# Performance work log

Measured on AMD Instinct MI355X. Metric: run time of the kernel, lower is better.

The kernel has to match this reference:

```python
import jax, jax.numpy as jnp
import numpy as np

B, N, D = 4, 2048, 1024
THRESHOLD_FACTOR = 1.25


def setup_inputs() -> dict:
    key = jax.random.key(0)
    ks = jax.random.split(key, 8)
    s = 0.02  # init scale matching torch.randn * 0.02
    return {
        "hidden_states": jax.random.normal(ks[0], (B, N, D), jnp.float32),
        "Wq": jax.random.normal(ks[1], (D, D), jnp.float32) * s,
        "bq": jnp.zeros((D,), jnp.float32),
        "Wk": jax.random.normal(ks[2], (D, D), jnp.float32) * s,
        "bk": jnp.zeros((D,), jnp.float32),
        "Wv": jax.random.normal(ks[3], (D, D), jnp.float32) * s,
        "bv": jnp.zeros((D,), jnp.float32),
        "Wo": jax.random.normal(ks[4], (D, D), jnp.float32) * s,
        "bo": jnp.zeros((D,), jnp.float32),
        "Wtq": jax.random.normal(ks[5], (2, D), jnp.float32) * s,  # nn.Linear(D, 2)
        "btq": jnp.zeros((2,), jnp.float32),
        "Wfq": jax.random.normal(ks[6], (D, 2), jnp.float32) * s,  # HebbianLinear(2, D)
        "bfq": jnp.zeros((D,), jnp.float32),
    }


def _linear(x, W, b):
    return x @ W.T + b


def reference(hidden_states, Wq, bq, Wk, bk, Wv, bv, Wo, bo, Wtq, btq, Wfq, bfq):
    d = hidden_states.shape[-1]
    q = _linear(hidden_states, Wq, bq)
    k = _linear(hidden_states, Wk, bk)
    v = _linear(hidden_states, Wv, bv)
    scores = jnp.einsum('bid,bjd->bij', q, k) / jnp.sqrt(jnp.asarray(d, scores_dtype := q.dtype))

    # PhaseAwareBinaryAttention on 2-d quantum projection
    qp = _linear(hidden_states, Wtq, btq)            # [B, N, 2]
    diff = qp[:, :, None, :] - qp[:, None, :, :]      # [B, N, N, 2]
    dist_sq = jnp.sum(diff * diff, axis=-1)           # [B, N, N]
    phase_diff = jnp.arctan2(diff[..., 1], diff[..., 0])
    forward_bias = 0.5 * (1.0 + jnp.cos(phase_diff))
    mean_dist = jnp.mean(dist_sq, axis=(-1, -2), keepdims=True)
    std_dist = jnp.std(dist_sq, axis=(-1, -2), keepdims=True, ddof=1)  # torch unbiased std
    threshold = mean_dist + THRESHOLD_FACTOR * std_dist
    n = dist_sq.shape[-1]
    causal = jnp.tril(jnp.ones((n, n), bool))
    valid = (dist_sq <= threshold) & causal[None]
    binary_attn = valid.astype(scores.dtype) * forward_bias

    masked = jnp.where(binary_attn == 0, -jnp.inf, scores)
    weights = jax.nn.softmax(masked, axis=-1)
    context = jnp.einsum('bij,bjd->bid', weights, v)
    output = _linear(context, Wo, bo)

    # F.normalize(qp, p=2, dim=-1) with eps=1e-12
    r_embed = qp / jnp.maximum(jnp.linalg.norm(qp, axis=-1, keepdims=True), 1e-12)
    quantum_output = _linear(r_embed, Wfq, bfq)
    return hidden_states + output + 0.1 * quantum_output
```

## Files before the change

### kernel.cpp

```cpp
#include <hip/hip_runtime.h>
#include <math.h>

#define N_TOK 2048
#define DIM   1024
#define BATCH 4

typedef float v4f  __attribute__((ext_vector_type(4)));
typedef __bf16 v8bf __attribute__((ext_vector_type(8)));
typedef unsigned short v8us __attribute__((ext_vector_type(8)));

static __device__ __forceinline__ unsigned short f2bf(float f) {
  unsigned int u = __float_as_uint(f);
  u += 0x7fffu + ((u >> 16) & 1u);
  return (unsigned short)(u >> 16);
}
static __device__ __forceinline__ float bf2f(unsigned short h) {
  return __uint_as_float((unsigned int)h << 16);
}

__global__ __launch_bounds__(256) void castqp_kernel(
    const float* __restrict__ hs, const float* __restrict__ Wtq,
    const float* __restrict__ btq, unsigned short* __restrict__ hs_b,
    float2* __restrict__ qp, float2* __restrict__ remb) {
  int w = threadIdx.x >> 6, lane = threadIdx.x & 63;
  int row = blockIdx.x * 4 + w;
  const float* x = hs + (size_t)row * DIM;
  unsigned short* d = hs_b + (size_t)row * DIM;
  float a0 = 0.f, a1 = 0.f;
#pragma unroll
  for (int it = 0; it < 4; ++it) {
    int base = it * 256 + lane * 4;
    float4 v = *(const float4*)(x + base);
    float4 w0 = *(const float4*)(Wtq + base);
    float4 w1 = *(const float4*)(Wtq + DIM + base);
    ushort4 pk;
    pk.x = f2bf(v.x); pk.y = f2bf(v.y); pk.z = f2bf(v.z); pk.w = f2bf(v.w);
    *(ushort4*)(d + base) = pk;
    a0 += v.x * w0.x + v.y * w0.y + v.z * w0.z + v.w * w0.w;
    a1 += v.x * w1.x + v.y * w1.y + v.z * w1.z + v.w * w1.w;
  }
  for (int o = 32; o; o >>= 1) { a0 += __shfl_xor(a0, o); a1 += __shfl_xor(a1, o); }
  if (lane == 0) {
    a0 += btq[0]; a1 += btq[1];
    qp[row] = make_float2(a0, a1);
    float nrm = fmaxf(sqrtf(a0 * a0 + a1 * a1), 1e-12f);
    remb[row] = make_float2(a0 / nrm, a1 / nrm);
  }
}

__global__ __launch_bounds__(256) void cast_w4_kernel(
    const float* __restrict__ W0, const float* __restrict__ W1,
    const float* __restrict__ W2, const float* __restrict__ W3,
    unsigned short* __restrict__ D0, unsigned short* __restrict__ D1,
    unsigned short* __restrict__ D2, unsigned short* __restrict__ D3) {
  const float* s;
  unsigned short* d;
  switch (blockIdx.y) {
    case 0: s = W0; d = D0; break;
    case 1: s = W1; d = D1; break;
    case 2: s = W2; d = D2; break;
    default: s = W3; d = D3; break;
  }
  int i = (blockIdx.x * 256 + threadIdx.x) * 4;
  float4 v = *(const float4*)(s + i);
  d[i + 0] = f2bf(v.x); d[i + 1] = f2bf(v.y);
  d[i + 2] = f2bf(v.z); d[i + 3] = f2bf(v.w);
}

__global__ __launch_bounds__(256) void moments_kernel(
    const float2* __restrict__ qp, double* __restrict__ part) {
  int b = blockIdx.y;
  int i0 = blockIdx.x * 32;
  const float2* qb = qp + ((size_t)b << 11);
  double s1 = 0.0, s2 = 0.0;
  for (int idx = threadIdx.x; idx < 32 * N_TOK; idx += 256) {
    int i = i0 + (idx >> 11), j = idx & (N_TOK - 1);
    float2 pi = qb[i], pj = qb[j];
    float dx = pi.x - pj.x, dy = pi.y - pj.y;
    float dd = __fadd_rn(__fmul_rn(dx, dx), __fmul_rn(dy, dy));
    s1 += (double)dd;
    s2 += (double)dd * (double)dd;
  }
  int lane = threadIdx.x & 63, w = threadIdx.x >> 6;
  for (int o = 32; o; o >>= 1) { s1 += __shfl_xor(s1, o); s2 += __shfl_xor(s2, o); }
  __shared__ double red[8];
  if (lane == 0) { red[w] = s1; red[4 + w] = s2; }
  __syncthreads();
  if (threadIdx.x == 0) {
    int slot = b * 64 + blockIdx.x;
    part[slot * 2 + 0] = red[0] + red[1] + red[2] + red[3];
    part[slot * 2 + 1] = red[4] + red[5] + red[6] + red[7];
  }
}

__global__ __launch_bounds__(256) void thr_kernel(
    const double* __restrict__ part, float* __restrict__ thr) {
  int b = threadIdx.x >> 6, lane = threadIdx.x & 63;
  double s1 = part[(b * 64 + lane) * 2 + 0];
  double s2 = part[(b * 64 + lane) * 2 + 1];
  for (int o = 32; o; o >>= 1) { s1 += __shfl_xor(s1, o); s2 += __shfl_xor(s2, o); }
  if (lane == 0) {
    double n2 = (double)N_TOK * (double)N_TOK;
    double mean = s1 / n2;
    double var = (s2 - n2 * mean * mean) / (n2 - 1.0);
    if (var < 0.0) var = 0.0;
    thr[b] = (float)(mean + 1.25 * sqrt(var));
  }
}

__device__ __forceinline__ void gemm_ktile_loop(
    const unsigned short* __restrict__ Ag, const unsigned short* __restrict__ Bg,
    int ldA, int ldB, int kBeg, int kEnd,
    unsigned short* As, unsigned short* Bs, v4f acc[4][4]) {
  const int tid  = threadIdx.x;
  const int lane = tid & 63;
  const int wm   = ((tid >> 6) & 1) << 6, wn = (tid >> 7) << 6;
  const int quad = lane >> 4, l16 = lane & 15;
  const int srow = tid >> 3;
  const int scol = ((tid ^ srow) & 7) * 8;
  for (int k0 = kBeg; k0 < kEnd; k0 += 64) {
    __syncthreads();
#pragma unroll
    for (int it = 0; it < 4; ++it) {
      int row = srow + it * 32;
      const unsigned short* ga = Ag + (size_t)row * ldA + k0 + scol;
      const unsigned short* gb = Bg + (size_t)row * ldB + k0 + scol;
      unsigned short* la = As + (size_t)(it * 256 + (tid & ~63)) * 8;
      unsigned short* lb = Bs + (size_t)(it * 256 + (tid & ~63)) * 8;
      __builtin_amdgcn_global_load_lds((const __attribute__((address_space(1))) void*)ga,
                                       (__attribute__((address_space(3))) void*)la, 16, 0, 0);
      __builtin_amdgcn_global_load_lds((const __attribute__((address_space(1))) void*)gb,
                                       (__attribute__((address_space(3))) void*)lb, 16, 0, 0);
    }
    asm volatile("s_waitcnt vmcnt(0)" ::: "memory");
    __syncthreads();
#pragma unroll
    for (int kk = 0; kk < 64; kk += 32) {
      const int co = ((((kk >> 3) + quad) ^ (l16 & 7)) << 3);
      v8bf af[4], bfv[4];
#pragma unroll
      for (int i = 0; i < 4; ++i)
        af[i] = *(const v8bf*)(As + (wm + i * 16 + l16) * 64 + co);
#pragma unroll
      for (int i = 0; i < 4; ++i)
        bfv[i] = *(const v8bf*)(Bs + (wn + i * 16 + l16) * 64 + co);
#pragma unroll
      for (int mi = 0; mi < 4; ++mi)
#pragma unroll
        for (int ni = 0; ni < 4; ++ni)
          acc[mi][ni] = __builtin_amdgcn_mfma_f32_16x16x32_bf16(af[mi], bfv[ni], acc[mi][ni], 0, 0, 0);
    }
  }
}

#define PROLOG128                                                     \
  __shared__ __attribute__((aligned(16))) unsigned short smem[2][128 * 64];\
  unsigned short* As = smem[0];                                       \
  unsigned short* Bs = smem[1];                                       \
  v4f acc[4][4];                                                      \
  _Pragma("unroll") for (int i_ = 0; i_ < 4; ++i_)                    \
  _Pragma("unroll") for (int j_ = 0; j_ < 4; ++j_)                    \
      acc[i_][j_] = v4f{0.f, 0.f, 0.f, 0.f};                          \
  const int lane = threadIdx.x & 63, w = threadIdx.x >> 6;            \
  const int wm = (w & 1) << 6, wn = (w >> 1) << 6;                    \
  const int quad = lane >> 4, l16 = lane & 15;

__global__ __launch_bounds__(256) void gemm_qkv_fused_kernel(
    const unsigned short* __restrict__ X, const unsigned short* __restrict__ Wqkv,
    const float* __restrict__ bq, const float* __restrict__ bk,
    const float* __restrict__ bv, unsigned short* __restrict__ q_b,
    unsigned short* __restrict__ k_b, unsigned short* __restrict__ v_t) {
  PROLOG128
  int lid = blockIdx.y * 24 + blockIdx.x;
  int xcd = lid & 7, slot = lid >> 3;
  int by = (xcd << 3) | (slot & 7);
  int bx = slot >> 3;
  int m0 = by * 128, n0 = bx * 128;
  gemm_ktile_loop(X + (size_t)m0 * DIM, Wqkv + (size_t)n0 * DIM, DIM, DIM, 0, DIM, As, Bs, acc);
  int region = n0 >> 10;
  const float* bias = region == 0 ? bq : region == 1 ? bk : bv;
  int cbase = n0 & 1023;
  if (region < 2) {
    unsigned short* dst = region == 0 ? q_b : k_b;
#pragma unroll
    for (int mi = 0; mi < 4; ++mi) {
      int row0 = m0 + wm + mi * 16 + quad * 4;
#pragma unroll
      for (int ni = 0; ni < 4; ++ni) {
        int col = cbase + wn + ni * 16 + l16;
        float bcol = bias[col];
#pragma unroll
        for (int r = 0; r < 4; ++r)
          dst[(size_t)(row0 + r) * DIM + col] = f2bf(acc[mi][ni][r] + bcol);
      }
    }
  } else {
    unsigned short* T = &smem[0][0];
    __syncthreads();
#pragma unroll
    for (int mi = 0; mi < 4; ++mi) {
      int trow = wm + mi * 16 + quad * 4;
#pragma unroll
      for (int ni = 0; ni < 4; ++ni) {
        int fcol = wn + ni * 16 + l16;
        float bcol = bias[cbase + fcol];
        ushort4 pk;
        pk.x = f2bf(acc[mi][ni][0] + bcol);
        pk.y = f2bf(acc[mi][ni][1] + bcol);
        pk.z = f2bf(acc[mi][ni][2] + bcol);
        pk.w = f2bf(acc[mi][ni][3] + bcol);
        *(ushort4*)(T + fcol * 128 + trow) = pk;
      }
    }
    __syncthreads();
    int bb = m0 >> 11, tok0 = m0 & (N_TOK - 1);
    unsigned short* dstb = v_t + ((size_t)(bb << 10) + cbase) * N_TOK + tok0;
#pragma unroll
    for (int kk2 = 0; kk2 < 8; ++kk2) {
      int c = kk2 * 256 + threadIdx.x;
      int f = c >> 4, e0 = (c & 15) * 8;
      v8us v = *(const v8us*)(T + f * 128 + e0);
      *(v8us*)(dstb + (size_t)f * N_TOK + e0) = v;
    }
  }
}

__global__ __launch_bounds__(256) void gemm_scores_kernel(
    const unsigned short* __restrict__ q, const unsigned short* __restrict__ k,
    const float2* __restrict__ qp, const float* __restrict__ thr,
    unsigned short* __restrict__ S) {
  PROLOG128
  int b = blockIdx.y;
  int lid = blockIdx.x;
  int t = (lid & 7) * 17 + (lid >> 3);
  int ti = (int)((sqrtf(8.f * (float)t + 1.f) - 1.f) * 0.5f);
  while ((ti + 1) * (ti + 2) / 2 <= t) ++ti;
  while (ti * (ti + 1) / 2 > t) --ti;
  int tj = t - ti * (ti + 1) / 2;
  int i0 = ti * 128, j0 = tj * 128;
  const unsigned short* qb = q + (size_t)b * N_TOK * DIM;
  const unsigned short* kb = k + (size_t)b * N_TOK * DIM;
  gemm_ktile_loop(qb + (size_t)i0 * DIM, kb + (size_t)j0 * DIM, DIM, DIM, 0, DIM, As, Bs, acc);
  float th = thr[b];
  const float2* qpb = qp + ((size_t)b << 11);
  unsigned short* Sb = S + (size_t)b * N_TOK * N_TOK;
  float2 pjv[4];
#pragma unroll
  for (int ni = 0; ni < 4; ++ni) pjv[ni] = qpb[j0 + wn + ni * 16 + l16];
#pragma unroll
  for (int mi = 0; mi < 4; ++mi) {
#pragma unroll
    for (int r = 0; r < 4; ++r) {
      int i = i0 + wm + mi * 16 + quad * 4 + r;
      float2 pi2 = qpb[i];
#pragma unroll
      for (int ni = 0; ni < 4; ++ni) {
        int j = j0 + wn + ni * 16 + l16;
        if (j <= i) {
          float dx = pi2.x - pjv[ni].x, dy = pi2.y - pjv[ni].y;
          float dd = __fadd_rn(__fmul_rn(dx, dx), __fmul_rn(dy, dy));
          bool ok = (dd <= th);
          if (ok && dx < 0.f && fabsf(dy) <= 3e-4f * (-dx)) {
            float fb = 0.5f * (1.f + cosf(atan2f(dy, dx)));
            if (fb == 0.f) ok = false;
          }
          Sb[(size_t)i * N_TOK + j] = ok ? f2bf(acc[mi][ni][r] * 0.03125f) : 0xFF80;
        }
      }
    }
  }
}

__global__ __launch_bounds__(256) void softmax_kernel(
    const unsigned short* __restrict__ S, unsigned short* __restrict__ P) {
  int row = blockIdx.x;
  int b = row >> 11, i = row & (N_TOK - 1);
  const unsigned short* s = S + ((size_t)b * N_TOK + i) * N_TOK;
  unsigned short* p = P + ((size_t)b * N_TOK + i) * N_TOK;
  int tid = threadIdx.x, lane = tid & 63, w = tid >> 6;
  int lim = i + 1;
  int tail0 = lim & ~7, ntail = lim - tail0;
  __shared__ float redmax[4], redsum[4];
  float mx = -__builtin_inff();
  for (int j = tid * 8; j + 8 <= lim; j += 2048) {
    v8us v = *(const v8us*)(s + j);
#pragma unroll
    for (int e = 0; e < 8; ++e) mx = fmaxf(mx, bf2f(v[e]));
  }
  if (tid < ntail) mx = fmaxf(mx, bf2f(s[tail0 + tid]));
  for (int o = 32; o; o >>= 1) mx = fmaxf(mx, __shfl_xor(mx, o));
  if (lane == 0) redmax[w] = mx;
  __syncthreads();
  mx = fmaxf(fmaxf(redmax[0], redmax[1]), fmaxf(redmax[2], redmax[3]));
  float sum = 0.f;
  for (int j = tid * 8; j + 8 <= lim; j += 2048) {
    v8us v = *(const v8us*)(s + j);
#pragma unroll
    for (int e = 0; e < 8; ++e) sum += __expf(bf2f(v[e]) - mx);
  }
  if (tid < ntail) sum += __expf(bf2f(s[tail0 + tid]) - mx);
  for (int o = 32; o; o >>= 1) sum += __shfl_xor(sum, o);
  if (lane == 0) redsum[w] = sum;
  __syncthreads();
  sum = redsum[0] + redsum[1] + redsum[2] + redsum[3];
  float inv = 1.f / sum;
  for (int j = tid * 8; j + 8 <= lim; j += 2048) {
    v8us v = *(const v8us*)(s + j);
    v8us o;
#pragma unroll
    for (int e = 0; e < 8; ++e) o[e] = f2bf(__expf(bf2f(v[e]) - mx) * inv);
    *(v8us*)(p + j) = o;
  }
  if (tid < ntail) p[tail0 + tid] = f2bf(__expf(bf2f(s[tail0 + tid]) - mx) * inv);
  int zs = (lim + 7) & ~7;
  if (tid < zs - lim) p[lim + tid] = 0;
  v8us zv;
#pragma unroll
  for (int e = 0; e < 8; ++e) zv[e] = 0;
  for (int j = zs + tid * 8; j < N_TOK; j += 2048) *(v8us*)(p + j) = zv;
}

__global__ __launch_bounds__(256) void gemm_pv_kernel(
    const unsigned short* __restrict__ P, const unsigned short* __restrict__ vt,
    unsigned short* __restrict__ ctx) {
  PROLOG128
  int b = blockIdx.z;
  int ti = blockIdx.y, d0 = blockIdx.x * 128;
  int i0 = ti * 128;
  const unsigned short* Pb = P + (size_t)b * N_TOK * N_TOK;
  const unsigned short* Vb = vt + ((size_t)b * DIM + d0) * N_TOK;
  int kEnd = (ti + 1) * 128;
  gemm_ktile_loop(Pb + (size_t)i0 * N_TOK, Vb, N_TOK, N_TOK, 0, kEnd, As, Bs, acc);
#pragma unroll
  for (int mi = 0; mi < 4; ++mi) {
    int row0 = i0 + wm + mi * 16 + quad * 4;
#pragma unroll
    for (int ni = 0; ni < 4; ++ni) {
      int d = d0 + wn + ni * 16 + l16;
#pragma unroll
      for (int r = 0; r < 4; ++r)
        ctx[((size_t)b * N_TOK + row0 + r) * DIM + d] = f2bf(acc[mi][ni][r]);
    }
  }
}

__global__ __launch_bounds__(256) void gemm_out_kernel(
    const unsigned short* __restrict__ ctx, const unsigned short* __restrict__ Wob,
    const float* __restrict__ bo, const float* __restrict__ hs,
    const float2* __restrict__ remb, const float* __restrict__ Wfq,
    const float* __restrict__ bfq, float* __restrict__ out) {
  PROLOG128
  int lid = blockIdx.y * 8 + blockIdx.x;
  int xcd = lid & 7, slot = lid >> 3;
  int by = (xcd << 3) | (slot & 7);
  int bx = slot >> 3;
  int m0 = by * 128, n0 = bx * 128;
  gemm_ktile_loop(ctx + (size_t)m0 * DIM, Wob + (size_t)n0 * DIM, DIM, DIM, 0, DIM, As, Bs, acc);
#pragma unroll
  for (int mi = 0; mi < 4; ++mi) {
    int row0 = m0 + wm + mi * 16 + quad * 4;
#pragma unroll
    for (int ni = 0; ni < 4; ++ni) {
      int col = n0 + wn + ni * 16 + l16;
      float bias2 = bo[col] + 0.1f * bfq[col];
      float wf0 = 0.1f * Wfq[col * 2 + 0], wf1 = 0.1f * Wfq[col * 2 + 1];
#pragma unroll
      for (int r = 0; r < 4; ++r) {
        int row = row0 + r;
        float2 re = remb[row];
        out[(size_t)row * DIM + col] =
            acc[mi][ni][r] + bias2 + hs[(size_t)row * DIM + col] + re.x * wf0 + re.y * wf1;
      }
    }
  }
}

extern "C" void kernel_launch(void* const* d_in, const int* in_sizes, int n_in,
                              void* d_out, int out_size, void* d_ws, size_t ws_size,
                              hipStream_t stream) {
  const float* hs  = (const float*)d_in[0];
  const float* Wq  = (const float*)d_in[1];
  const float* bq  = (const float*)d_in[2];
  const float* Wk  = (const float*)d_in[3];
  const float* bk  = (const float*)d_in[4];
  const float* Wv  = (const float*)d_in[5];
  const float* bv  = (const float*)d_in[6];
  const float* Wo  = (const float*)d_in[7];
  const float* bo  = (const float*)d_in[8];
  const float* Wtq = (const float*)d_in[9];
  const float* btq = (const float*)d_in[10];
  const float* Wfq = (const float*)d_in[11];
  const float* bfq = (const float*)d_in[12];
  float* out = (float*)d_out;

  char* ws = (char*)d_ws;
  size_t off = 0;
  auto alloc = [&](size_t bytes) {
    char* p = ws + off;
    off += (bytes + 255) & ~(size_t)255;
    return p;
  };
  unsigned short* hs_b = (unsigned short*)alloc((size_t)8192 * 1024 * 2);
  unsigned short* q_b  = (unsigned short*)alloc((size_t)8192 * 1024 * 2);
  unsigned short* k_b  = (unsigned short*)alloc((size_t)8192 * 1024 * 2);
  unsigned short* v_t  = (unsigned short*)alloc((size_t)8192 * 1024 * 2);
  unsigned short* Wq_b = (unsigned short*)alloc((size_t)1024 * 1024 * 2);
  unsigned short* Wk_b = (unsigned short*)alloc((size_t)1024 * 1024 * 2);
  unsigned short* Wv_b = (unsigned short*)alloc((size_t)1024 * 1024 * 2);
  unsigned short* Wo_b = (unsigned short*)alloc((size_t)1024 * 1024 * 2);
  float2* qp   = (float2*)alloc((size_t)8192 * 8);
  float2* remb = (float2*)alloc((size_t)8192 * 8);
  double* part = (double*)alloc((size_t)BATCH * 64 * 2 * 8);
  float*  thr  = (float*)alloc(64);
  unsigned short* S = (unsigned short*)alloc((size_t)BATCH * N_TOK * N_TOK * 2);
  unsigned short* P   = q_b;
  unsigned short* ctx = hs_b;

  castqp_kernel<<<2048, 256, 0, stream>>>(hs, Wtq, btq, hs_b, qp, remb);
  cast_w4_kernel<<<dim3(1024, 4), 256, 0, stream>>>(Wq, Wk, Wv, Wo, Wq_b, Wk_b, Wv_b, Wo_b);
  moments_kernel<<<dim3(64, BATCH), 256, 0, stream>>>((const float2*)qp, part);
  thr_kernel<<<1, 256, 0, stream>>>(part, thr);

  gemm_qkv_fused_kernel<<<dim3(24, 64), 256, 0, stream>>>(
      hs_b, Wq_b, bq, bk, bv, q_b, k_b, v_t);

  gemm_scores_kernel<<<dim3(136, 4), 256, 0, stream>>>(
      q_b, k_b, (const float2*)qp, thr, S);

  softmax_kernel<<<8192, 256, 0, stream>>>(S, P);

  gemm_pv_kernel<<<dim3(8, 16, 4), 256, 0, stream>>>(P, v_t, ctx);

  gemm_out_kernel<<<dim3(8, 64), 256, 0, stream>>>(ctx, Wo_b, bo, hs, remb, Wfq, bfq, out);
}
```

Before: 382.0 us.

## Double-buffer LDS tiles with async global-to-LDS loads in scores, PV, out GEMMs

Measured after the change: 370.5 us. -3.0%, faster.

```diff
diff --git a/kernel.cpp b/kernel.cpp
--- a/kernel.cpp
+++ b/kernel.cpp
@@ -153,10 +153,85 @@
   }
 }
 
+__device__ __forceinline__ void ktile_compute128(
+    const unsigned short* As, const unsigned short* Bs,
+    int wm, int wn, int quad, int l16, v4f acc[4][4]) {
+#pragma unroll
+  for (int kk = 0; kk < 64; kk += 32) {
+    const int co = ((((kk >> 3) + quad) ^ (l16 & 7)) << 3);
+    v8bf af[4], bfv[4];
+#pragma unroll
+    for (int i = 0; i < 4; ++i)
+      af[i] = *(const v8bf*)(As + (wm + i * 16 + l16) * 64 + co);
+#pragma unroll
+    for (int i = 0; i < 4; ++i)
+      bfv[i] = *(const v8bf*)(Bs + (wn + i * 16 + l16) * 64 + co);
+#pragma unroll
+    for (int mi = 0; mi < 4; ++mi)
+#pragma unroll
+      for (int ni = 0; ni < 4; ++ni)
+        acc[mi][ni] = __builtin_amdgcn_mfma_f32_16x16x32_bf16(af[mi], bfv[ni], acc[mi][ni], 0, 0, 0);
+  }
+}
+
+__device__ __forceinline__ void gemm_ktile_loop_db(
+    const unsigned short* __restrict__ Ag, const unsigned short* __restrict__ Bg,
+    int ldA, int ldB, int kEnd,
+    unsigned short* As0, unsigned short* Bs0,
+    unsigned short* As1, unsigned short* Bs1, v4f acc[4][4]) {
+  const int tid  = threadIdx.x;
+  const int lane = tid & 63;
+  const int wm   = ((tid >> 6) & 1) << 6, wn = (tid >> 7) << 6;
+  const int quad = lane >> 4, l16 = lane & 15;
+  const int srow = tid >> 3;
+  const int scol = ((tid ^ srow) & 7) * 8;
+  const unsigned short* gA = Ag + (size_t)srow * ldA + scol;
+  const unsigned short* gB = Bg + (size_t)srow * ldB + scol;
+  const int lbase = (tid & ~63) * 8;
+
+  auto stage = [&](unsigned short* As, unsigned short* Bs, int k0) {
+#pragma unroll
+    for (int it = 0; it < 4; ++it) {
+      const unsigned short* ga = gA + (size_t)(it * 32) * ldA + k0;
+      const unsigned short* gb = gB + (size_t)(it * 32) * ldB + k0;
+      unsigned short* la = As + it * 2048 + lbase;
+      unsigned short* lb = Bs + it * 2048 + lbase;
+      __builtin_amdgcn_global_load_lds((const __attribute__((address_space(1))) void*)ga,
+                                       (__attribute__((address_space(3))) void*)la, 16, 0, 0);
+      __builtin_amdgcn_global_load_lds((const __attribute__((address_space(1))) void*)gb,
+                                       (__attribute__((address_space(3))) void*)lb, 16, 0, 0);
+    }
+  };
+
+  stage(As0, Bs0, 0);
+  asm volatile("s_waitcnt vmcnt(0)" ::: "memory");
+  __syncthreads();
+  for (int k0 = 0; k0 < kEnd; k0 += 128) {
+    stage(As1, Bs1, k0 + 64);
+    ktile_compute128(As0, Bs0, wm, wn, quad, l16, acc);
+    asm volatile("s_waitcnt vmcnt(0)" ::: "memory");
+    __syncthreads();
+    if (k0 + 128 < kEnd) stage(As0, Bs0, k0 + 128);
+    ktile_compute128(As1, Bs1, wm, wn, quad, l16, acc);
+    asm volatile("s_waitcnt vmcnt(0)" ::: "memory");
+    __syncthreads();
+  }
+}
+
 #define PROLOG128                                                     \
   __shared__ __attribute__((aligned(16))) unsigned short smem[2][128 * 64];\
   unsigned short* As = smem[0];                                       \
   unsigned short* Bs = smem[1];                                       \
+  v4f acc[4][4];                                                      \
+  _Pragma("unroll") for (int i_ = 0; i_ < 4; ++i_)                    \
+  _Pragma("unroll") for (int j_ = 0; j_ < 4; ++j_)                    \
+      acc[i_][j_] = v4f{0.f, 0.f, 0.f, 0.f};                          \
+  const int lane = threadIdx.x & 63, w = threadIdx.x >> 6;            \
+  const int wm = (w & 1) << 6, wn = (w >> 1) << 6;                    \
+  const int quad = lane >> 4, l16 = lane & 15;
+
+#define PROLOG128DB                                                   \
+  __shared__ __attribute__((aligned(16))) unsigned short smem[4][128 * 64];\
   v4f acc[4][4];                                                      \
   _Pragma("unroll") for (int i_ = 0; i_ < 4; ++i_)                    \
   _Pragma("unroll") for (int j_ = 0; j_ < 4; ++j_)                    \
@@ -229,7 +304,7 @@
     const unsigned short* __restrict__ q, const unsigned short* __restrict__ k,
     const float2* __restrict__ qp, const float* __restrict__ thr,
     unsigned short* __restrict__ S) {
-  PROLOG128
+  PROLOG128DB
   int b = blockIdx.y;
   int lid = blockIdx.x;
   int t = (lid & 7) * 17 + (lid >> 3);
@@ -240,7 +315,8 @@
   int i0 = ti * 128, j0 = tj * 128;
   const unsigned short* qb = q + (size_t)b * N_TOK * DIM;
   const unsigned short* kb = k + (size_t)b * N_TOK * DIM;
-  gemm_ktile_loop(qb + (size_t)i0 * DIM, kb + (size_t)j0 * DIM, DIM, DIM, 0, DIM, As, Bs, acc);
+  gemm_ktile_loop_db(qb + (size_t)i0 * DIM, kb + (size_t)j0 * DIM, DIM, DIM, DIM,
+                     smem[0], smem[1], smem[2], smem[3], acc);
   float th = thr[b];
   const float2* qpb = qp + ((size_t)b << 11);
   unsigned short* Sb = S + (size_t)b * N_TOK * N_TOK;
@@ -323,14 +399,15 @@
 __global__ __launch_bounds__(256) void gemm_pv_kernel(
     const unsigned short* __restrict__ P, const unsigned short* __restrict__ vt,
     unsigned short* __restrict__ ctx) {
-  PROLOG128
+  PROLOG128DB
   int b = blockIdx.z;
   int ti = blockIdx.y, d0 = blockIdx.x * 128;
   int i0 = ti * 128;
   const unsigned short* Pb = P + (size_t)b * N_TOK * N_TOK;
   const unsigned short* Vb = vt + ((size_t)b * DIM + d0) * N_TOK;
   int kEnd = (ti + 1) * 128;
-  gemm_ktile_loop(Pb + (size_t)i0 * N_TOK, Vb, N_TOK, N_TOK, 0, kEnd, As, Bs, acc);
+  gemm_ktile_loop_db(Pb + (size_t)i0 * N_TOK, Vb, N_TOK, N_TOK, kEnd,
+                     smem[0], smem[1], smem[2], smem[3], acc);
 #pragma unroll
   for (int mi = 0; mi < 4; ++mi) {
     int row0 = i0 + wm + mi * 16 + quad * 4;
@@ -349,13 +426,14 @@
     const float* __restrict__ bo, const float* __restrict__ hs,
     const float2* __restrict__ remb, const float* __restrict__ Wfq,
     const float* __restrict__ bfq, float* __restrict__ out) {
-  PROLOG128
+  PROLOG128DB
   int lid = blockIdx.y * 8 + blockIdx.x;
   int xcd = lid & 7, slot = lid >> 3;
   int by = (xcd << 3) | (slot & 7);
   int bx = slot >> 3;
   int m0 = by * 128, n0 = bx * 128;
-  gemm_ktile_loop(ctx + (size_t)m0 * DIM, Wob + (size_t)n0 * DIM, DIM, DIM, 0, DIM, As, Bs, acc);
+  gemm_ktile_loop_db(ctx + (size_t)m0 * DIM, Wob + (size_t)n0 * DIM, DIM, DIM, DIM,
+                     smem[0], smem[1], smem[2], smem[3], acc);
 #pragma unroll
   for (int mi = 0; mi < 4; ++mi) {
     int row0 = m0 + wm + mi * 16 + quad * 4;
```
